# Optimization experiments

Measured on AMD Instinct MI355X. Metric: run time of the kernel, lower is better.

The kernel has to match this reference:

```python
import jax, jax.numpy as jnp
import numpy as np

MAX_DISPLACEMENT = 4


def setup_inputs() -> dict:
    key = jax.random.key(0)
    k1, k2 = jax.random.split(key)
    B, C, H, W = 8, 128, 128, 256
    features1 = jax.random.normal(k1, (B, C, H, W), dtype=jnp.float32)
    features2 = jax.random.normal(k2, (B, C, H, W), dtype=jnp.float32)
    return {"features1": features1, "features2": features2}


def _cost_volume(features1, features2, max_displacement):
    B, C, H, W = features1.shape
    d = max_displacement
    # zero-pad features2 spatially by d (uflow compute_cost_volume semantics)
    padded = jnp.pad(features2, ((0, 0), (0, 0), (d, d), (d, d)))
    num_shifts = 2 * d + 1
    costs = []
    for i in range(num_shifts):          # fixed small structural loop: (2d+1)^2 = 81
        for j in range(num_shifts):
            shifted = jax.lax.dynamic_slice(padded, (0, 0, i, j), (B, C, H, W))
            # mean over channel dim of elementwise product
            costs.append(jnp.mean(features1 * shifted, axis=1))
    return jnp.stack(costs, axis=1)  # [B, (2d+1)^2, H, W]


def reference(features1, features2):
    return _cost_volume(features1, features2, MAX_DISPLACEMENT)
```

## Files before the change

### kernel.cpp

```cpp
#include <hip/hip_runtime.h>

#define B_  8
#define C_  128
#define H_  128
#define W_  256
#define HW_ (H_ * W_)
#define TH  8
#define TW  32
#define S2S 40
#define S1S 40
#define S1OFF (16 * S2S)
#define PAIRN (S1OFF + TH * S1S)
#define NTHREADS 576

typedef __fp16 h2 __attribute__((ext_vector_type(2)));

__device__ __forceinline__ float dot2f16(unsigned int a, unsigned int b, float c) {
#if __has_builtin(__builtin_amdgcn_fdot2)
    return __builtin_amdgcn_fdot2(__builtin_bit_cast(h2, a),
                                  __builtin_bit_cast(h2, b), c, false);
#else
    h2 ha = __builtin_bit_cast(h2, a), hb = __builtin_bit_cast(h2, b);
    return c + (float)ha.x * (float)hb.x + (float)ha.y * (float)hb.y;
#endif
}

__device__ __forceinline__ unsigned int pk(float x, float y) {
    h2 r = __builtin_amdgcn_cvt_pkrtz(x, y);
    return __builtin_bit_cast(unsigned int, r);
}

__global__ __launch_bounds__(NTHREADS, 3) void cv_kernel(
    const float* __restrict__ f1g, const float* __restrict__ f2g,
    float* __restrict__ outg) {
    __shared__ __align__(16) unsigned int lds[2][2][PAIRN];

    const int tid = threadIdx.x;
    const int w0 = blockIdx.x * TW;
    const int h0 = blockIdx.y * TH;
    const int b  = blockIdx.z;

    const bool stg = (tid < 448);
    int off0 = 0, ld0 = 0, pp = 0;
    float m0 = 0.f;
    const float* p0 = f1g;
    if (tid < 320) {
        pp = tid / 160;
        int slot = tid % 160;
        int r = slot / 10, c4 = slot % 10;
        int gh = h0 - 4 + r, gw = w0 - 4 + 4 * c4;
        bool valid = (gh >= 0) && (gh < H_) && (gw >= 0) && (gw <= W_ - 4);
        int ghc = min(max(gh, 0), H_ - 1);
        int gwc = min(max(gw, 0), W_ - 4);
        off0 = ((b * C_ + 2 * pp) * H_ + ghc) * W_ + gwc;
        p0   = f2g;
        ld0  = r * S2S + 4 * c4;
        m0   = valid ? 1.f : 0.f;
    } else if (tid < 448) {
        int u = tid - 320;
        pp = u / 64;
        int slot = u % 64;
        int r = slot / 8, c4 = slot % 8;
        off0 = ((b * C_ + 2 * pp) * H_ + h0 + r) * W_ + w0 + 4 * c4;
        p0   = f1g;
        ld0  = S1OFF + r * S1S + 4 * c4;
        m0   = 1.f;
    }

#define LOADST(Sa, Sb)                                                        \
    do {                                                                      \
        if (stg) {                                                            \
            Sa = *(const float4*)(p0 + off0);                                 \
            Sb = *(const float4*)(p0 + off0 + HW_);                           \
            off0 += 4 * HW_;                                                  \
        }                                                                     \
    } while (0)

#define STOREST(bi, Sa, Sb)                                                   \
    do {                                                                      \
        if (stg) {                                                            \
            uint4 wv;                                                         \
            wv.x = pk(Sa.x * m0, Sb.x * m0);                                  \
            wv.y = pk(Sa.y * m0, Sb.y * m0);                                  \
            wv.z = pk(Sa.z * m0, Sb.z * m0);                                  \
            wv.w = pk(Sa.w * m0, Sb.w * m0);                                  \
            *(uint4*)(&lds[bi][pp][ld0]) = wv;                                \
        }                                                                     \
    } while (0)

#define BAR()                                                                 \
    do {                                                                      \
        asm volatile("s_waitcnt lgkmcnt(0)" ::: "memory");                    \
        __builtin_amdgcn_s_barrier();                                         \
    } while (0)

    const int di   = tid >> 6;
    const int lane = tid & 63;
    const int hh   = lane >> 3;
    const int sc   = lane & 7;
    const int rdF2 = (hh + di) * S2S + 4 * sc;
    const int rdF1 = S1OFF + hh * S1S + 4 * sc;

    float acc[9][4];
#pragma unroll
    for (int j = 0; j < 9; ++j)
#pragma unroll
        for (int p = 0; p < 4; ++p) acc[j][p] = 0.f;

#define COMPUTE(bi)                                                           \
    do {                                                                      \
        _Pragma("unroll")                                                     \
        for (int q = 0; q < 2; ++q) {                                         \
            const unsigned int* buf = lds[bi][q];                             \
            uint4 fa = *(const uint4*)(buf + rdF2);                           \
            uint4 fb = *(const uint4*)(buf + rdF2 + 4);                       \
            uint4 fc = *(const uint4*)(buf + rdF2 + 8);                       \
            uint4 ga = *(const uint4*)(buf + rdF1);                           \
            unsigned int f2u[12] = {fa.x, fa.y, fa.z, fa.w, fb.x, fb.y,       \
                                    fb.z, fb.w, fc.x, fc.y, fc.z, fc.w};      \
            unsigned int f1u[4]  = {ga.x, ga.y, ga.z, ga.w};                  \
            _Pragma("unroll")                                                 \
            for (int j = 0; j < 9; ++j)                                       \
                _Pragma("unroll")                                             \
                for (int p = 0; p < 4; ++p)                                   \
                    acc[j][p] = dot2f16(f1u[p], f2u[p + j], acc[j][p]);       \
        }                                                                     \
    } while (0)

    float4 aA, bA, aB, bB;

    LOADST(aA, bA);
    LOADST(aB, bB);
    STOREST(0, aA, bA);
    BAR();

    for (int s = 0; s < 30; s += 2) {
        LOADST(aA, bA);
        COMPUTE(0);
        STOREST(1, aB, bB);
        BAR();
        LOADST(aB, bB);
        COMPUTE(1);
        STOREST(0, aA, bA);
        BAR();
    }
    COMPUTE(0);
    STOREST(1, aB, bB);
    BAR();
    COMPUTE(1);

    const float inv = 1.0f / 128.0f;
    int obase = ((b * 81 + di * 9) * H_ + h0 + hh) * W_ + w0 + 4 * sc;
#pragma unroll
    for (int j = 0; j < 9; ++j) {
        float4 o = make_float4(acc[j][0] * inv, acc[j][1] * inv,
                               acc[j][2] * inv, acc[j][3] * inv);
        *(float4*)(outg + obase) = o;
        obase += HW_;
    }
}

extern "C" void kernel_launch(void* const* d_in, const int* in_sizes, int n_in,
                              void* d_out, int out_size, void* d_ws, size_t ws_size,
                              hipStream_t stream) {
    const float* f1 = (const float*)d_in[0];
    const float* f2 = (const float*)d_in[1];
    float* out = (float*)d_out;
    dim3 grid(W_ / TW, H_ / TH, B_);
    cv_kernel<<<grid, NTHREADS, 0, stream>>>(f1, f2, out);
}
```

Measured before the change: 155.1 us.

## Read features1 directly from global per thread and stage 8 channels per LDS step

Features1 is no longer staged through LDS. Each compute thread loads its own features1 values from global memory and packs them to fp16 in registers. Only features2 halos are staged, now 4 channel pairs (8 channels) per barrier step, which halves the number of barriers. All 576 threads share the staging work, with the first 64 taking a second slot. The LDS row layout is padded (PU skew, 48-word rows) to reduce bank conflicts. The trade-off is more global load latency exposed inside the compute loop and higher register pressure from the doubled staging.

```diff
diff --git a/kernel.cpp b/kernel.cpp
--- a/kernel.cpp
+++ b/kernel.cpp
@@ -7,10 +7,10 @@
 #define HW_ (H_ * W_)
 #define TH  8
 #define TW  32
-#define S2S 40
-#define S1S 40
-#define S1OFF (16 * S2S)
-#define PAIRN (S1OFF + TH * S1S)
+#define NPAIR 4
+#define ROWD 48
+#define PAIRN (16 * ROWD)
+#define PU(u) ((u) + ((u) >> 3))
 #define NTHREADS 576
 
 typedef __fp16 h2 __attribute__((ext_vector_type(2)));
@@ -33,58 +33,68 @@
 __global__ __launch_bounds__(NTHREADS, 3) void cv_kernel(
     const float* __restrict__ f1g, const float* __restrict__ f2g,
     float* __restrict__ outg) {
-    __shared__ __align__(16) unsigned int lds[2][2][PAIRN];
+    __shared__ __align__(16) unsigned int lds[2][NPAIR * PAIRN];
 
     const int tid = threadIdx.x;
     const int w0 = blockIdx.x * TW;
     const int h0 = blockIdx.y * TH;
     const int b  = blockIdx.z;
 
-    const bool stg = (tid < 448);
-    int off0 = 0, ld0 = 0, pp = 0;
-    float m0 = 0.f;
-    const float* p0 = f1g;
-    if (tid < 320) {
-        pp = tid / 160;
-        int slot = tid % 160;
-        int r = slot / 10, c4 = slot % 10;
-        int gh = h0 - 4 + r, gw = w0 - 4 + 4 * c4;
+    int offA, ldA, offB = 0, ldB = 0;
+    float mA, mB = 0.f;
+    const bool dual = (tid < 64);
+    {
+        int s = tid;
+        int pp = s / 160, rem = s % 160;
+        int r = rem / 10, cu = rem % 10;
+        int gh = h0 - 4 + r, gw = w0 - 4 + 4 * cu;
         bool valid = (gh >= 0) && (gh < H_) && (gw >= 0) && (gw <= W_ - 4);
         int ghc = min(max(gh, 0), H_ - 1);
         int gwc = min(max(gw, 0), W_ - 4);
-        off0 = ((b * C_ + 2 * pp) * H_ + ghc) * W_ + gwc;
-        p0   = f2g;
-        ld0  = r * S2S + 4 * c4;
-        m0   = valid ? 1.f : 0.f;
-    } else if (tid < 448) {
-        int u = tid - 320;
-        pp = u / 64;
-        int slot = u % 64;
-        int r = slot / 8, c4 = slot % 8;
-        off0 = ((b * C_ + 2 * pp) * H_ + h0 + r) * W_ + w0 + 4 * c4;
-        p0   = f1g;
-        ld0  = S1OFF + r * S1S + 4 * c4;
-        m0   = 1.f;
+        offA = ((b * C_ + 2 * pp) * H_ + ghc) * W_ + gwc;
+        ldA  = pp * PAIRN + r * ROWD + 4 * PU(cu);
+        mA   = valid ? 1.f : 0.f;
+    }
+    if (dual) {
+        int s = 576 + tid;
+        int pp = s / 160, rem = s % 160;
+        int r = rem / 10, cu = rem % 10;
+        int gh = h0 - 4 + r, gw = w0 - 4 + 4 * cu;
+        bool valid = (gh >= 0) && (gh < H_) && (gw >= 0) && (gw <= W_ - 4);
+        int ghc = min(max(gh, 0), H_ - 1);
+        int gwc = min(max(gw, 0), W_ - 4);
+        offB = ((b * C_ + 2 * pp) * H_ + ghc) * W_ + gwc;
+        ldB  = pp * PAIRN + r * ROWD + 4 * PU(cu);
+        mB   = valid ? 1.f : 0.f;
     }
 
-#define LOADST(Sa, Sb)                                                        \
+#define LOADST()                                                              \
     do {                                                                      \
-        if (stg) {                                                            \
-            Sa = *(const float4*)(p0 + off0);                                 \
-            Sb = *(const float4*)(p0 + off0 + HW_);                           \
-            off0 += 4 * HW_;                                                  \
+        aA = *(const float4*)(f2g + offA);                                    \
+        bA = *(const float4*)(f2g + offA + HW_);                              \
+        offA += 8 * HW_;                                                      \
+        if (dual) {                                                           \
+            aB = *(const float4*)(f2g + offB);                                \
+            bB = *(const float4*)(f2g + offB + HW_);                          \
+            offB += 8 * HW_;                                                  \
         }                                                                     \
     } while (0)
 
-#define STOREST(bi, Sa, Sb)                                                   \
+#define STOREST(bi)                                                           \
     do {                                                                      \
-        if (stg) {                                                            \
-            uint4 wv;                                                         \
-            wv.x = pk(Sa.x * m0, Sb.x * m0);                                  \
-            wv.y = pk(Sa.y * m0, Sb.y * m0);                                  \
-            wv.z = pk(Sa.z * m0, Sb.z * m0);                                  \
-            wv.w = pk(Sa.w * m0, Sb.w * m0);                                  \
-            *(uint4*)(&lds[bi][pp][ld0]) = wv;                                \
+        uint4 wv;                                                             \
+        wv.x = pk(aA.x * mA, bA.x * mA);                                      \
+        wv.y = pk(aA.y * mA, bA.y * mA);                                      \
+        wv.z = pk(aA.z * mA, bA.z * mA);                                      \
+        wv.w = pk(aA.w * mA, bA.w * mA);                                      \
+        *(uint4*)(&lds[bi][ldA]) = wv;                                        \
+        if (dual) {                                                           \
+            uint4 w2;                                                         \
+            w2.x = pk(aB.x * mB, bB.x * mB);                                  \
+            w2.y = pk(aB.y * mB, bB.y * mB);                                  \
+            w2.z = pk(aB.z * mB, bB.z * mB);                                  \
+            w2.w = pk(aB.w * mB, bB.w * mB);                                  \
+            *(uint4*)(&lds[bi][ldB]) = w2;                                    \
         }                                                                     \
     } while (0)
 
@@ -98,8 +108,11 @@
     const int lane = tid & 63;
     const int hh   = lane >> 3;
     const int sc   = lane & 7;
-    const int rdF2 = (hh + di) * S2S + 4 * sc;
-    const int rdF1 = S1OFF + hh * S1S + 4 * sc;
+    int rdm[3];
+#pragma unroll
+    for (int m = 0; m < 3; ++m)
+        rdm[m] = (hh + di) * ROWD + 4 * PU(sc + m);
+    int off1 = (b * C_ * H_ + h0 + hh) * W_ + w0 + 4 * sc;
 
     float acc[9][4];
 #pragma unroll
@@ -110,42 +123,48 @@
 #define COMPUTE(bi)                                                           \
     do {                                                                      \
         _Pragma("unroll")                                                     \
-        for (int q = 0; q < 2; ++q) {                                         \
-            const unsigned int* buf = lds[bi][q];                             \
-            uint4 fa = *(const uint4*)(buf + rdF2);                           \
-            uint4 fb = *(const uint4*)(buf + rdF2 + 4);                       \
-            uint4 fc = *(const uint4*)(buf + rdF2 + 8);                       \
-            uint4 ga = *(const uint4*)(buf + rdF1);                           \
+        for (int q = 0; q < NPAIR; ++q) {                                     \
+            float4 x = *(const float4*)(f1g + off1 + (2 * q) * HW_);          \
+            float4 y = *(const float4*)(f1g + off1 + (2 * q + 1) * HW_);      \
+            const unsigned int* buf = &lds[bi][q * PAIRN];                    \
+            uint4 fa = *(const uint4*)(buf + rdm[0]);                         \
+            uint4 fb = *(const uint4*)(buf + rdm[1]);                         \
+            uint4 fc = *(const uint4*)(buf + rdm[2]);                         \
+            unsigned int fy[4];                                               \
+            fy[0] = pk(x.x, y.x);                                             \
+            fy[1] = pk(x.y, y.y);                                             \
+            fy[2] = pk(x.z, y.z);                                             \
+            fy[3] = pk(x.w, y.w);                                             \
             unsigned int f2u[12] = {fa.x, fa.y, fa.z, fa.w, fb.x, fb.y,       \
                                     fb.z, fb.w, fc.x, fc.y, fc.z, fc.w};      \
-            unsigned int f1u[4]  = {ga.x, ga.y, ga.z, ga.w};                  \
             _Pragma("unroll")                                                 \
             for (int j = 0; j < 9; ++j)                                       \
                 _Pragma("unroll")                                             \
                 for (int p = 0; p < 4; ++p)                                   \
-                    acc[j][p] = dot2f16(f1u[p], f2u[p + j], acc[j][p]);       \
+                    acc[j][p] = dot2f16(fy[p], f2u[p + j], acc[j][p]);        \
         }                                                                     \
+        off1 += 2 * NPAIR * HW_;                                              \
     } while (0)
 
     float4 aA, bA, aB, bB;
 
-    LOADST(aA, bA);
-    LOADST(aB, bB);
-    STOREST(0, aA, bA);
+    LOADST();
+    STOREST(0);
     BAR();
 
-    for (int s = 0; s < 30; s += 2) {
-        LOADST(aA, bA);
+    for (int st = 0; st < 14; st += 2) {
+        LOADST();
         COMPUTE(0);
-        STOREST(1, aB, bB);
+        STOREST(1);
         BAR();
-        LOADST(aB, bB);
+        LOADST();
         COMPUTE(1);
-        STOREST(0, aA, bA);
+        STOREST(0);
         BAR();
     }
+    LOADST();
     COMPUTE(0);
-    STOREST(1, aB, bB);
+    STOREST(1);
     BAR();
     COMPUTE(1);
 
```

After: 507.7 us. 227% more time.

## Compute cost volume with MFMA 16x16x32 f16 matrix products

Applied to the files above, without the earlier changes.

Replaces per-thread packed fp16 dot products with MFMA matrix multiplies. Each wavefront handles one output row and forms a 16-pixel by 32-column product of f1 against shifted f2 rows, then keeps only the band of outputs inside the 9 horizontal offsets. The f1 fragment is held in registers and f2 is staged in LDS with 8 channels per load. This trades extra MFMA work on unused off-band products, plus scattered scalar output stores, for much higher matrix-unit throughput.

```diff
diff --git a/kernel.cpp b/kernel.cpp
--- a/kernel.cpp
+++ b/kernel.cpp
@@ -6,87 +6,95 @@
 #define W_  256
 #define HW_ (H_ * W_)
 #define TH  8
-#define TW  32
-#define S2S 40
-#define S1S 40
-#define S1OFF (16 * S2S)
-#define PAIRN (S1OFF + TH * S1S)
-#define NTHREADS 576
+#define TW  16
+#define SROW 392
+#define BUFN 6400
+#define NTHREADS 512
 
+typedef __fp16 h8 __attribute__((ext_vector_type(8)));
 typedef __fp16 h2 __attribute__((ext_vector_type(2)));
+typedef float  f4 __attribute__((ext_vector_type(4)));
 
-__device__ __forceinline__ float dot2f16(unsigned int a, unsigned int b, float c) {
-#if __has_builtin(__builtin_amdgcn_fdot2)
-    return __builtin_amdgcn_fdot2(__builtin_bit_cast(h2, a),
-                                  __builtin_bit_cast(h2, b), c, false);
-#else
-    h2 ha = __builtin_bit_cast(h2, a), hb = __builtin_bit_cast(h2, b);
-    return c + (float)ha.x * (float)hb.x + (float)ha.y * (float)hb.y;
-#endif
+__device__ __forceinline__ unsigned pk(float x, float y) {
+    h2 r = __builtin_amdgcn_cvt_pkrtz(x, y);
+    return __builtin_bit_cast(unsigned, r);
 }
 
-__device__ __forceinline__ unsigned int pk(float x, float y) {
-    h2 r = __builtin_amdgcn_cvt_pkrtz(x, y);
-    return __builtin_bit_cast(unsigned int, r);
-}
-
-__global__ __launch_bounds__(NTHREADS, 3) void cv_kernel(
+__global__ __launch_bounds__(NTHREADS, 2) void cv_kernel(
     const float* __restrict__ f1g, const float* __restrict__ f2g,
     float* __restrict__ outg) {
-    __shared__ __align__(16) unsigned int lds[2][2][PAIRN];
+    __shared__ __align__(16) unsigned lds[2 * BUFN];
 
-    const int tid = threadIdx.x;
-    const int w0 = blockIdx.x * TW;
-    const int h0 = blockIdx.y * TH;
-    const int b  = blockIdx.z;
+    const int tid  = threadIdx.x;
+    const int w0   = blockIdx.x * TW;
+    const int h0   = blockIdx.y * TH;
+    const int b    = blockIdx.z;
+    const int wid  = tid >> 6;
+    const int lane = tid & 63;
+    const int an   = lane & 15;
+    const int ag   = lane >> 4;
+    const int h    = h0 + wid;
 
-    const bool stg = (tid < 448);
-    int off0 = 0, ld0 = 0, pp = 0;
-    float m0 = 0.f;
-    const float* p0 = f1g;
-    if (tid < 320) {
-        pp = tid / 160;
-        int slot = tid % 160;
-        int r = slot / 10, c4 = slot % 10;
-        int gh = h0 - 4 + r, gw = w0 - 4 + 4 * c4;
+    const bool stg = (tid < 384);
+    int offS = 0, ldS = 0, uS = 0;
+    float mS = 0.f;
+    if (stg) {
+        int cgS = tid / 96;
+        int rem = tid % 96;
+        int r = rem / 6;  uS = rem % 6;
+        int gh = h0 - 4 + r, gw = w0 - 4 + 4 * uS;
         bool valid = (gh >= 0) && (gh < H_) && (gw >= 0) && (gw <= W_ - 4);
         int ghc = min(max(gh, 0), H_ - 1);
         int gwc = min(max(gw, 0), W_ - 4);
-        off0 = ((b * C_ + 2 * pp) * H_ + ghc) * W_ + gwc;
-        p0   = f2g;
-        ld0  = r * S2S + 4 * c4;
-        m0   = valid ? 1.f : 0.f;
-    } else if (tid < 448) {
-        int u = tid - 320;
-        pp = u / 64;
-        int slot = u % 64;
-        int r = slot / 8, c4 = slot % 8;
-        off0 = ((b * C_ + 2 * pp) * H_ + h0 + r) * W_ + w0 + 4 * c4;
-        p0   = f1g;
-        ld0  = S1OFF + r * S1S + 4 * c4;
-        m0   = 1.f;
+        offS = (b * C_ + 8 * cgS) * HW_ + ghc * W_ + gwc;
+        ldS  = r * SROW + 4 * cgS;
+        mS   = valid ? 1.f : 0.f;
     }
 
-#define LOADST(Sa, Sb)                                                        \
+    uint4 afr[4];
+    {
+        int offA = (b * C_ + 8 * ag) * HW_ + h * W_ + w0 + an;
+#pragma unroll
+        for (int kb = 0; kb < 4; ++kb) {
+            float v0 = f1g[offA];            float v1 = f1g[offA + HW_];
+            float v2 = f1g[offA + 2 * HW_];  float v3 = f1g[offA + 3 * HW_];
+            float v4 = f1g[offA + 4 * HW_];  float v5 = f1g[offA + 5 * HW_];
+            float v6 = f1g[offA + 6 * HW_];  float v7 = f1g[offA + 7 * HW_];
+            afr[kb] = make_uint4(pk(v0, v1), pk(v2, v3), pk(v4, v5), pk(v6, v7));
+            offA += 32 * HW_;
+        }
+    }
+
+    float4 sA, sB, sC, sD, sE, sF, sG, sH;
+
+#define LOADST()                                                              \
+    do { if (stg) {                                                           \
+        sA = *(const float4*)(f2g + offS);                                    \
+        sB = *(const float4*)(f2g + offS + HW_);                              \
+        sC = *(const float4*)(f2g + offS + 2 * HW_);                          \
+        sD = *(const float4*)(f2g + offS + 3 * HW_);                          \
+        sE = *(const float4*)(f2g + offS + 4 * HW_);                          \
+        sF = *(const float4*)(f2g + offS + 5 * HW_);                          \
+        sG = *(const float4*)(f2g + offS + 6 * HW_);                          \
+        sH = *(const float4*)(f2g + offS + 7 * HW_);                          \
+        offS += 32 * HW_;                                                     \
+    } } while (0)
+
+#define STQ(bofs, j, c0, c1, c2, c3, c4, c5, c6, c7)                          \
     do {                                                                      \
-        if (stg) {                                                            \
-            Sa = *(const float4*)(p0 + off0);                                 \
-            Sb = *(const float4*)(p0 + off0 + HW_);                           \
-            off0 += 4 * HW_;                                                  \
-        }                                                                     \
+        uint4 v;                                                              \
+        v.x = pk(c0 * mS, c1 * mS); v.y = pk(c2 * mS, c3 * mS);               \
+        v.z = pk(c4 * mS, c5 * mS); v.w = pk(c6 * mS, c7 * mS);               \
+        *(uint4*)(&lds[(bofs) + ldS + (4 * uS + (j)) * 16]) = v;              \
     } while (0)
 
-#define STOREST(bi, Sa, Sb)                                                   \
-    do {                                                                      \
-        if (stg) {                                                            \
-            uint4 wv;                                                         \
-            wv.x = pk(Sa.x * m0, Sb.x * m0);                                  \
-            wv.y = pk(Sa.y * m0, Sb.y * m0);                                  \
-            wv.z = pk(Sa.z * m0, Sb.z * m0);                                  \
-            wv.w = pk(Sa.w * m0, Sb.w * m0);                                  \
-            *(uint4*)(&lds[bi][pp][ld0]) = wv;                                \
-        }                                                                     \
-    } while (0)
+#define STOREST(bi)                                                           \
+    do { if (stg) {                                                           \
+        STQ((bi) * BUFN, 0, sA.x, sB.x, sC.x, sD.x, sE.x, sF.x, sG.x, sH.x);  \
+        STQ((bi) * BUFN, 1, sA.y, sB.y, sC.y, sD.y, sE.y, sF.y, sG.y, sH.y);  \
+        STQ((bi) * BUFN, 2, sA.z, sB.z, sC.z, sD.z, sE.z, sF.z, sG.z, sH.z);  \
+        STQ((bi) * BUFN, 3, sA.w, sB.w, sC.w, sD.w, sE.w, sF.w, sG.w, sH.w);  \
+    } } while (0)
 
 #define BAR()                                                                 \
     do {                                                                      \
@@ -94,69 +102,49 @@
         __builtin_amdgcn_s_barrier();                                         \
     } while (0)
 
-    const int di   = tid >> 6;
-    const int lane = tid & 63;
-    const int hh   = lane >> 3;
-    const int sc   = lane & 7;
-    const int rdF2 = (hh + di) * S2S + 4 * sc;
-    const int rdF1 = S1OFF + hh * S1S + 4 * sc;
+    f4 acc[9][2];
+#pragma unroll
+    for (int di = 0; di < 9; ++di) {
+        f4 z = {0.f, 0.f, 0.f, 0.f};
+        acc[di][0] = z; acc[di][1] = z;
+    }
 
-    float acc[9][4];
-#pragma unroll
-    for (int j = 0; j < 9; ++j)
-#pragma unroll
-        for (int p = 0; p < 4; ++p) acc[j][p] = 0.f;
-
-#define COMPUTE(bi)                                                           \
+#define COMPUTE(bi, kb)                                                       \
     do {                                                                      \
+        const int bo = (bi) * BUFN + an * 16 + 4 * ag;                        \
         _Pragma("unroll")                                                     \
-        for (int q = 0; q < 2; ++q) {                                         \
-            const unsigned int* buf = lds[bi][q];                             \
-            uint4 fa = *(const uint4*)(buf + rdF2);                           \
-            uint4 fb = *(const uint4*)(buf + rdF2 + 4);                       \
-            uint4 fc = *(const uint4*)(buf + rdF2 + 8);                       \
-            uint4 ga = *(const uint4*)(buf + rdF1);                           \
-            unsigned int f2u[12] = {fa.x, fa.y, fa.z, fa.w, fb.x, fb.y,       \
-                                    fb.z, fb.w, fc.x, fc.y, fc.z, fc.w};      \
-            unsigned int f1u[4]  = {ga.x, ga.y, ga.z, ga.w};                  \
-            _Pragma("unroll")                                                 \
-            for (int j = 0; j < 9; ++j)                                       \
-                _Pragma("unroll")                                             \
-                for (int p = 0; p < 4; ++p)                                   \
-                    acc[j][p] = dot2f16(f1u[p], f2u[p + j], acc[j][p]);       \
+        for (int di = 0; di < 9; ++di) {                                      \
+            int ba = bo + (wid + di) * SROW;                                  \
+            h8 b0 = *(const h8*)(&lds[ba]);                                   \
+            h8 b1 = *(const h8*)(&lds[ba + 256]);                             \
+            acc[di][0] = __builtin_amdgcn_mfma_f32_16x16x32_f16(              \
+                __builtin_bit_cast(h8, afr[kb]), b0, acc[di][0], 0, 0, 0);    \
+            acc[di][1] = __builtin_amdgcn_mfma_f32_16x16x32_f16(              \
+                __builtin_bit_cast(h8, afr[kb]), b1, acc[di][1], 0, 0, 0);    \
         }                                                                     \
     } while (0)
 
-    float4 aA, bA, aB, bB;
-
-    LOADST(aA, bA);
-    LOADST(aB, bB);
-    STOREST(0, aA, bA);
-    BAR();
-
-    for (int s = 0; s < 30; s += 2) {
-        LOADST(aA, bA);
-        COMPUTE(0);
-        STOREST(1, aB, bB);
-        BAR();
-        LOADST(aB, bB);
-        COMPUTE(1);
-        STOREST(0, aA, bA);
-        BAR();
-    }
-    COMPUTE(0);
-    STOREST(1, aB, bB);
-    BAR();
-    COMPUTE(1);
+    LOADST(); STOREST(0); BAR();
+    LOADST(); COMPUTE(0, 0); STOREST(1); BAR();
+    LOADST(); COMPUTE(1, 1); STOREST(0); BAR();
+    LOADST(); COMPUTE(0, 2); STOREST(1); BAR();
+    COMPUTE(1, 3);
 
     const float inv = 1.0f / 128.0f;
-    int obase = ((b * 81 + di * 9) * H_ + h0 + hh) * W_ + w0 + 4 * sc;
+    const int m  = 4 * ag;
+    const int ob = (b * 81 * H_ + h) * W_ + w0 + m;
 #pragma unroll
-    for (int j = 0; j < 9; ++j) {
-        float4 o = make_float4(acc[j][0] * inv, acc[j][1] * inv,
-                               acc[j][2] * inv, acc[j][3] * inv);
-        *(float4*)(outg + obase) = o;
-        obase += HW_;
+    for (int di = 0; di < 9; ++di) {
+#pragma unroll
+        for (int t = 0; t < 2; ++t) {
+#pragma unroll
+            for (int j = 0; j < 4; ++j) {
+                int dj = 16 * t + an - m - j;
+                if ((unsigned)dj <= 8u) {
+                    outg[ob + (di * 9 + dj) * HW_ + j] = acc[di][t][j] * inv;
+                }
+            }
+        }
     }
 }
 
```

Measured after the change: 176.7 us. 1.14x slower.
